# Performance work log

Hardware: AMD Instinct MI355X
Metric: run time of the kernel (lower is better)

## Reference

```python
import jax, jax.numpy as jnp
import numpy as np

TAU = 0.1

def setup_inputs() -> dict:
    key = jax.random.key(0)
    kZ, k1, k2 = jax.random.split(key, 3)
    N, D = 8192, 128
    scale = 1.0 / np.sqrt(D)
    return {
        "Z": jax.random.normal(kZ, (N, D), dtype=jnp.float32),
        "W1": jax.random.normal(k1, (D, D), dtype=jnp.float32) * scale,
        "b1": jnp.zeros((D,), dtype=jnp.float32),
        "W2": jax.random.normal(k2, (D, D), dtype=jnp.float32) * scale,
        "b2": jnp.zeros((D,), dtype=jnp.float32),
    }

def reference(Z, W1, b1, W2, b2):
    # DiffusivityTransform: 2-layer MLP with ReLU (torch Linear: x @ W.T + b;
    # here W1/W2 are stored already transposed as [in, out])
    t = jax.nn.relu(Z @ W1 + b1) @ W2 + b2          # [N, D]
    sim = t @ t.T                                     # [N, N]
    S = jax.nn.softmax(sim, axis=1)                   # row-stochastic [N, N]
    Z_prop = S @ Z                                    # [N, D]
    return Z + TAU * (Z_prop - Z)
```

## Files before the change

kernel.cpp:

```cpp
#include <hip/hip_runtime.h>

typedef _Float16 half_t;
typedef _Float16 hx8 __attribute__((ext_vector_type(8)));
typedef _Float16 hx4 __attribute__((ext_vector_type(4)));
typedef float fx4 __attribute__((ext_vector_type(4)));

#define LOG2E 1.44269504088896f
#define TAU 0.1f
#define NSPLIT 8

__global__ __launch_bounds__(256) void mlpz_kernel(
    const float* __restrict__ Z, const float* __restrict__ W1,
    const float* __restrict__ b1, const float* __restrict__ W2,
    const float* __restrict__ b2, half_t* __restrict__ T,
    half_t* __restrict__ Zth)
{
  __shared__ float Ztile[16*132];
  __shared__ half_t Hs[16*136];
  const int tid = threadIdx.x;
  const int w = tid >> 6, lane = tid & 63;
  const int q = lane >> 4, c = lane & 15;
  const int rb = blockIdx.x*16;

#pragma unroll
  for (int i=0;i<2;++i) {
    int fid = i*256 + tid;
    int r = fid >> 5, c4 = (fid & 31)*4;
    *(fx4*)(&Ztile[r*132 + c4]) = *(const fx4*)(Z + (size_t)(rb + r)*128 + c4);
  }
  __syncthreads();

  {
    const int d = tid & 127, h = tid >> 7;
    hx8 hv;
#pragma unroll
    for (int u=0;u<8;++u) hv[u] = (half_t)Ztile[(h*8 + u)*132 + d];
    *(hx8*)(Zth + (size_t)d*8192 + rb + h*8) = hv;
  }

  hx8 zb[4];
#pragma unroll
  for (int ks=0;ks<4;++ks) {
    fx4 a = *(const fx4*)(&Ztile[c*132 + ks*32 + q*8]);
    fx4 b = *(const fx4*)(&Ztile[c*132 + ks*32 + q*8 + 4]);
#pragma unroll
    for (int u=0;u<4;++u) { zb[ks][u] = (half_t)a[u]; zb[ks][4+u] = (half_t)b[u]; }
  }

#pragma unroll
  for (int m2=0;m2<2;++m2) {
    const int mt = w*2 + m2;
    fx4 acc = (fx4){0.f,0.f,0.f,0.f};
#pragma unroll
    for (int ks=0;ks<4;++ks) {
      hx8 aw;
#pragma unroll
      for (int j=0;j<8;++j)
        aw[j] = (half_t)W1[(size_t)(ks*32 + q*8 + j)*128 + mt*16 + c];
      acc = __builtin_amdgcn_mfma_f32_16x16x32_f16(aw, zb[ks], acc, 0,0,0);
    }
    fx4 bias = *(const fx4*)(b1 + mt*16 + 4*q);
    hx4 hv;
#pragma unroll
    for (int i=0;i<4;++i) {
      float h = acc[i] + bias[i];
      hv[i] = (half_t)(h > 0.f ? h : 0.f);
    }
    *(hx4*)(&Hs[c*136 + mt*16 + 4*q]) = hv;
  }
  __syncthreads();

  hx8 hb[4];
#pragma unroll
  for (int ks=0;ks<4;++ks) hb[ks] = *(const hx8*)(&Hs[c*136 + ks*32 + q*8]);
#pragma unroll
  for (int m2=0;m2<2;++m2) {
    const int mt = w*2 + m2;
    fx4 acc = (fx4){0.f,0.f,0.f,0.f};
#pragma unroll
    for (int ks=0;ks<4;++ks) {
      hx8 aw;
#pragma unroll
      for (int j=0;j<8;++j)
        aw[j] = (half_t)W2[(size_t)(ks*32 + q*8 + j)*128 + mt*16 + c];
      acc = __builtin_amdgcn_mfma_f32_16x16x32_f16(aw, hb[ks], acc, 0,0,0);
    }
    fx4 bias = *(const fx4*)(b2 + mt*16 + 4*q);
    hx4 tv;
#pragma unroll
    for (int i=0;i<4;++i) tv[i] = (half_t)(acc[i] + bias[i]);
    *(hx4*)(T + (size_t)(rb + c)*128 + mt*16 + 4*q) = tv;
  }
}

__global__ __launch_bounds__(256,2) void flash_kernel(
    const half_t* __restrict__ T, const half_t* __restrict__ Zt,
    half_t* __restrict__ Pacc, float* __restrict__ Pm, float* __restrict__ Pl)
{
  __shared__ half_t Tbuf[2][8*512];
  __shared__ half_t Zbuf[2][8*512];
  const int tid = threadIdx.x;
  const int w = tid >> 6, lane = tid & 63;
  const int q = lane >> 4, c = lane & 15;
  const int bx = blockIdx.x;
  const int qb = bx >> 3, kh = bx & 7;
  const int wrow = qb*128 + w*32;
  const int sw = (c & 3) * 8;

  hx8 bq[2][4];
#pragma unroll
  for (int nt=0;nt<2;++nt)
#pragma unroll
    for (int ks=0;ks<4;++ks)
      bq[nt][ks] = *(const hx8*)(T + (size_t)(wrow + nt*16 + c)*128 + ks*32 + q*8);

  fx4 oacc[8][2];
#pragma unroll
  for (int mtd=0;mtd<8;++mtd)
#pragma unroll
    for (int nt=0;nt<2;++nt) oacc[mtd][nt] = (fx4){0.f,0.f,0.f,0.f};
  float m_run[2] = {-1e30f,-1e30f};
  float l_run[2] = {0.f,0.f};

  const int kbase = kh*1024;

  auto issue_loads = [&](int kt0, int b) {
    if (w < 2) {
#pragma unroll
      for (int i=0;i<4;++i) {
        int f = w*4 + i, mt = f >> 2, ks = f & 3;
        const half_t* gp = T + (size_t)(kt0 + mt*16 + c)*128 + ks*32 + q*8;
        half_t* lp = &Tbuf[b][f*512 + lane*8];
        __builtin_amdgcn_global_load_lds(
            (const __attribute__((address_space(1))) void*)gp,
            (__attribute__((address_space(3))) void*)lp, 16, 0, 0);
      }
    } else {
#pragma unroll
      for (int i=0;i<4;++i) {
        int f2 = (w-2)*4 + i;
        const half_t* gp = Zt + (size_t)(f2*16 + c)*8192 + kt0 + q*8;
        half_t* lp = &Zbuf[b][f2*512 + lane*8];
        __builtin_amdgcn_global_load_lds(
            (const __attribute__((address_space(1))) void*)gp,
            (__attribute__((address_space(3))) void*)lp, 16, 0, 0);
      }
    }
  };

  issue_loads(kbase, 0);

  for (int t=0;t<32;++t) {
    const int cur = t & 1;
    __syncthreads();
    half_t* Tcur = Tbuf[cur];
    half_t* Zcur = Zbuf[cur];
    half_t* Psw  = &Tbuf[cur][w*1024];

    fx4 sacc[2][2];
#pragma unroll
    for (int mt=0;mt<2;++mt)
#pragma unroll
      for (int nt=0;nt<2;++nt) sacc[mt][nt] = (fx4){0.f,0.f,0.f,0.f};
#pragma unroll
    for (int ks=0;ks<4;++ks)
#pragma unroll
      for (int mt=0;mt<2;++mt) {
        hx8 ak = *(const hx8*)(&Tcur[(mt*4+ks)*512 + lane*8]);
        sacc[mt][0] = __builtin_amdgcn_mfma_f32_16x16x32_f16(ak, bq[0][ks], sacc[mt][0], 0,0,0);
        sacc[mt][1] = __builtin_amdgcn_mfma_f32_16x16x32_f16(ak, bq[1][ks], sacc[mt][1], 0,0,0);
      }

    hx4 pk[2][2];
#pragma unroll
    for (int nt=0;nt<2;++nt) {
      float mx = -1e30f;
#pragma unroll
      for (int mt=0;mt<2;++mt)
#pragma unroll
        for (int i=0;i<4;++i) mx = fmaxf(mx, sacc[mt][nt][i]);
      mx = fmaxf(mx, __shfl_xor(mx, 16, 64));
      mx = fmaxf(mx, __shfl_xor(mx, 32, 64));
      float mnew = fmaxf(m_run[nt], mx);
      float alpha = __builtin_amdgcn_exp2f((m_run[nt]-mnew)*LOG2E);
      m_run[nt] = mnew;
      float nb = mnew*LOG2E;
      float rs = 0.f;
#pragma unroll
      for (int mt=0;mt<2;++mt) {
#pragma unroll
        for (int i=0;i<4;++i) {
          float p = __builtin_amdgcn_exp2f(sacc[mt][nt][i]*LOG2E - nb);
          rs += p;
          pk[nt][mt][i] = (half_t)p;
        }
      }
      rs += __shfl_xor(rs, 16, 64);
      rs += __shfl_xor(rs, 32, 64);
      l_run[nt] = l_run[nt]*alpha + rs;
#pragma unroll
      for (int mtd=0;mtd<8;++mtd)
#pragma unroll
        for (int i=0;i<4;++i) oacc[mtd][nt][i] *= alpha;
    }

    __syncthreads();
    if (t < 31) issue_loads(kbase + (t+1)*32, cur ^ 1);

#pragma unroll
    for (int nt=0;nt<2;++nt)
#pragma unroll
      for (int mt=0;mt<2;++mt)
        *(hx4*)(&Psw[(nt*16 + c)*32 + ((mt*16 + 4*q) ^ sw)]) = pk[nt][mt];

    {
      hx8 bp0 = *(const hx8*)(&Psw[(c     )*32 + ((q*8) ^ sw)]);
      hx8 bp1 = *(const hx8*)(&Psw[(16 + c)*32 + ((q*8) ^ sw)]);
#pragma unroll
      for (int mtd=0;mtd<8;++mtd) {
        hx8 az = *(const hx8*)(&Zcur[mtd*512 + lane*8]);
        oacc[mtd][0] = __builtin_amdgcn_mfma_f32_16x16x32_f16(az, bp0, oacc[mtd][0], 0,0,0);
        oacc[mtd][1] = __builtin_amdgcn_mfma_f32_16x16x32_f16(az, bp1, oacc[mtd][1], 0,0,0);
      }
    }
  }

#pragma unroll
  for (int nt=0;nt<2;++nt) {
    float inv = 1.0f / l_run[nt];
    const size_t rowg = (size_t)(bx*128 + w*32 + nt*16 + c);
#pragma unroll
    for (int mtd=0;mtd<8;++mtd) {
      hx4 ov;
#pragma unroll
      for (int i=0;i<4;++i) ov[i] = (half_t)(oacc[mtd][nt][i]*inv);
      *(hx4*)(Pacc + rowg*128 + mtd*16 + 4*q) = ov;
    }
    if (q == 0) {
      Pm[rowg] = m_run[nt];
      Pl[rowg] = l_run[nt];
    }
  }
}

__global__ __launch_bounds__(256) void merge_kernel(
    const float* __restrict__ Z, const half_t* __restrict__ Pacc,
    const float* __restrict__ Pm, const float* __restrict__ Pl,
    float* __restrict__ out)
{
  const int th = blockIdx.x*256 + threadIdx.x;
  const int r = th >> 5, cg = th & 31;
  const int qb = r >> 7, rr = r & 127;
  float mk[NSPLIT], lk[NSPLIT];
  float M = -1e30f;
#pragma unroll
  for (int k=0;k<NSPLIT;++k) {
    int p = qb*NSPLIT + k;
    mk[k] = Pm[p*128 + rr];
    lk[k] = Pl[p*128 + rr];
    M = fmaxf(M, mk[k]);
  }
  float L = 0.f, wk[NSPLIT];
#pragma unroll
  for (int k=0;k<NSPLIT;++k) { wk[k] = lk[k]*__builtin_amdgcn_exp2f((mk[k]-M)*LOG2E); L += wk[k]; }
  float o0=0.f,o1=0.f,o2=0.f,o3=0.f;
#pragma unroll
  for (int k=0;k<NSPLIT;++k) {
    int p = qb*NSPLIT + k;
    hx4 v = *(const hx4*)(Pacc + ((size_t)p*128 + rr)*128 + cg*4);
    o0 += wk[k]*(float)v[0]; o1 += wk[k]*(float)v[1];
    o2 += wk[k]*(float)v[2]; o3 += wk[k]*(float)v[3];
  }
  float invL = 1.0f / L;
  fx4 zv = *(const fx4*)(Z + (size_t)r*128 + cg*4);
  fx4 res;
  res[0] = (1.f-TAU)*zv[0] + TAU*o0*invL;
  res[1] = (1.f-TAU)*zv[1] + TAU*o1*invL;
  res[2] = (1.f-TAU)*zv[2] + TAU*o2*invL;
  res[3] = (1.f-TAU)*zv[3] + TAU*o3*invL;
  *(fx4*)(out + (size_t)r*128 + cg*4) = res;
}

extern "C" void kernel_launch(void* const* d_in, const int* in_sizes, int n_in,
                              void* d_out, int out_size, void* d_ws, size_t ws_size,
                              hipStream_t stream) {
  const float* Z  = (const float*)d_in[0];
  const float* W1 = (const float*)d_in[1];
  const float* b1 = (const float*)d_in[2];
  const float* W2 = (const float*)d_in[3];
  const float* b2 = (const float*)d_in[4];
  float* out = (float*)d_out;

  char* ws = (char*)d_ws;
  const size_t NBLK = 64 * NSPLIT;
  half_t* Thi  = (half_t*)(ws);
  half_t* Zth  = (half_t*)(ws + (size_t)2*1024*1024);
  half_t* Pacc = (half_t*)(ws + (size_t)4*1024*1024);
  float*  Pm   = (float*)(ws + (size_t)4*1024*1024 + NBLK*128*128*2);
  float*  Pl   = Pm + NBLK*128;

  hipLaunchKernelGGL(mlpz_kernel,  dim3(512),  dim3(256), 0, stream, Z, W1, b1, W2, b2, Thi, Zth);
  hipLaunchKernelGGL(flash_kernel, dim3(NBLK), dim3(256), 0, stream, Thi, Zth, Pacc, Pm, Pl);
  hipLaunchKernelGGL(merge_kernel, dim3(1024), dim3(256), 0, stream, Z, Pacc, Pm, Pl, out);
}
```

Before: 138.9 us.

## Halve query rows per flash block to double grid size and add MFMA priority

Result: slower. 144.8 us (+4.2%).

```diff
diff --git a/kernel.cpp b/kernel.cpp
--- a/kernel.cpp
+++ b/kernel.cpp
@@ -104,23 +104,19 @@
   const int q = lane >> 4, c = lane & 15;
   const int bx = blockIdx.x;
   const int qb = bx >> 3, kh = bx & 7;
-  const int wrow = qb*128 + w*32;
-  const int sw = (c & 3) * 8;
-
-  hx8 bq[2][4];
-#pragma unroll
-  for (int nt=0;nt<2;++nt)
-#pragma unroll
-    for (int ks=0;ks<4;++ks)
-      bq[nt][ks] = *(const hx8*)(T + (size_t)(wrow + nt*16 + c)*128 + ks*32 + q*8);
-
-  fx4 oacc[8][2];
-#pragma unroll
-  for (int mtd=0;mtd<8;++mtd)
-#pragma unroll
-    for (int nt=0;nt<2;++nt) oacc[mtd][nt] = (fx4){0.f,0.f,0.f,0.f};
-  float m_run[2] = {-1e30f,-1e30f};
-  float l_run[2] = {0.f,0.f};
+  const int wrow = qb*64 + w*16;
+  const int sw = (c & 7) * 8;
+
+  hx8 bq[4];
+#pragma unroll
+  for (int ks=0;ks<4;++ks)
+    bq[ks] = *(const hx8*)(T + (size_t)(wrow + c)*128 + ks*32 + q*8);
+
+  fx4 oacc[8];
+#pragma unroll
+  for (int mtd=0;mtd<8;++mtd) oacc[mtd] = (fx4){0.f,0.f,0.f,0.f};
+  float m_run = -1e30f;
+  float l_run = 0.f;
 
   const int kbase = kh*1024;
 
@@ -157,89 +153,79 @@
     half_t* Zcur = Zbuf[cur];
     half_t* Psw  = &Tbuf[cur][w*1024];
 
-    fx4 sacc[2][2];
-#pragma unroll
-    for (int mt=0;mt<2;++mt)
-#pragma unroll
-      for (int nt=0;nt<2;++nt) sacc[mt][nt] = (fx4){0.f,0.f,0.f,0.f};
+    fx4 sacc[2];
+#pragma unroll
+    for (int mt=0;mt<2;++mt) sacc[mt] = (fx4){0.f,0.f,0.f,0.f};
+    __builtin_amdgcn_s_setprio(1);
 #pragma unroll
     for (int ks=0;ks<4;++ks)
 #pragma unroll
       for (int mt=0;mt<2;++mt) {
         hx8 ak = *(const hx8*)(&Tcur[(mt*4+ks)*512 + lane*8]);
-        sacc[mt][0] = __builtin_amdgcn_mfma_f32_16x16x32_f16(ak, bq[0][ks], sacc[mt][0], 0,0,0);
-        sacc[mt][1] = __builtin_amdgcn_mfma_f32_16x16x32_f16(ak, bq[1][ks], sacc[mt][1], 0,0,0);
-      }
-
-    hx4 pk[2][2];
-#pragma unroll
-    for (int nt=0;nt<2;++nt) {
-      float mx = -1e30f;
-#pragma unroll
-      for (int mt=0;mt<2;++mt)
-#pragma unroll
-        for (int i=0;i<4;++i) mx = fmaxf(mx, sacc[mt][nt][i]);
-      mx = fmaxf(mx, __shfl_xor(mx, 16, 64));
-      mx = fmaxf(mx, __shfl_xor(mx, 32, 64));
-      float mnew = fmaxf(m_run[nt], mx);
-      float alpha = __builtin_amdgcn_exp2f((m_run[nt]-mnew)*LOG2E);
-      m_run[nt] = mnew;
-      float nb = mnew*LOG2E;
-      float rs = 0.f;
-#pragma unroll
-      for (int mt=0;mt<2;++mt) {
-#pragma unroll
-        for (int i=0;i<4;++i) {
-          float p = __builtin_amdgcn_exp2f(sacc[mt][nt][i]*LOG2E - nb);
-          rs += p;
-          pk[nt][mt][i] = (half_t)p;
-        }
-      }
-      rs += __shfl_xor(rs, 16, 64);
-      rs += __shfl_xor(rs, 32, 64);
-      l_run[nt] = l_run[nt]*alpha + rs;
-#pragma unroll
-      for (int mtd=0;mtd<8;++mtd)
-#pragma unroll
-        for (int i=0;i<4;++i) oacc[mtd][nt][i] *= alpha;
-    }
+        sacc[mt] = __builtin_amdgcn_mfma_f32_16x16x32_f16(ak, bq[ks], sacc[mt], 0,0,0);
+      }
+    __builtin_amdgcn_s_setprio(0);
+
+    float mx = -1e30f;
+#pragma unroll
+    for (int mt=0;mt<2;++mt)
+#pragma unroll
+      for (int i=0;i<4;++i) mx = fmaxf(mx, sacc[mt][i]);
+    mx = fmaxf(mx, __shfl_xor(mx, 16, 64));
+    mx = fmaxf(mx, __shfl_xor(mx, 32, 64));
+    float mnew = fmaxf(m_run, mx);
+    float alpha = __builtin_amdgcn_exp2f((m_run - mnew)*LOG2E);
+    m_run = mnew;
+    float nb = mnew*LOG2E;
+    float rs = 0.f;
+    hx4 pk[2];
+#pragma unroll
+    for (int mt=0;mt<2;++mt)
+#pragma unroll
+      for (int i=0;i<4;++i) {
+        float p = __builtin_amdgcn_exp2f(sacc[mt][i]*LOG2E - nb);
+        rs += p;
+        pk[mt][i] = (half_t)p;
+      }
+    rs += __shfl_xor(rs, 16, 64);
+    rs += __shfl_xor(rs, 32, 64);
+    l_run = l_run*alpha + rs;
+#pragma unroll
+    for (int mtd=0;mtd<8;++mtd)
+#pragma unroll
+      for (int i=0;i<4;++i) oacc[mtd][i] *= alpha;
 
     __syncthreads();
     if (t < 31) issue_loads(kbase + (t+1)*32, cur ^ 1);
 
 #pragma unroll
-    for (int nt=0;nt<2;++nt)
-#pragma unroll
-      for (int mt=0;mt<2;++mt)
-        *(hx4*)(&Psw[(nt*16 + c)*32 + ((mt*16 + 4*q) ^ sw)]) = pk[nt][mt];
+    for (int mt=0;mt<2;++mt)
+      *(hx4*)(&Psw[c*64 + ((mt*16 + 4*q) ^ sw)]) = pk[mt];
 
     {
-      hx8 bp0 = *(const hx8*)(&Psw[(c     )*32 + ((q*8) ^ sw)]);
-      hx8 bp1 = *(const hx8*)(&Psw[(16 + c)*32 + ((q*8) ^ sw)]);
+      hx8 bp = *(const hx8*)(&Psw[c*64 + ((q*8) ^ sw)]);
+      __builtin_amdgcn_s_setprio(1);
 #pragma unroll
       for (int mtd=0;mtd<8;++mtd) {
         hx8 az = *(const hx8*)(&Zcur[mtd*512 + lane*8]);
-        oacc[mtd][0] = __builtin_amdgcn_mfma_f32_16x16x32_f16(az, bp0, oacc[mtd][0], 0,0,0);
-        oacc[mtd][1] = __builtin_amdgcn_mfma_f32_16x16x32_f16(az, bp1, oacc[mtd][1], 0,0,0);
-      }
-    }
-  }
-
-#pragma unroll
-  for (int nt=0;nt<2;++nt) {
-    float inv = 1.0f / l_run[nt];
-    const size_t rowg = (size_t)(bx*128 + w*32 + nt*16 + c);
-#pragma unroll
-    for (int mtd=0;mtd<8;++mtd) {
-      hx4 ov;
-#pragma unroll
-      for (int i=0;i<4;++i) ov[i] = (half_t)(oacc[mtd][nt][i]*inv);
-      *(hx4*)(Pacc + rowg*128 + mtd*16 + 4*q) = ov;
-    }
-    if (q == 0) {
-      Pm[rowg] = m_run[nt];
-      Pl[rowg] = l_run[nt];
-    }
+        oacc[mtd] = __builtin_amdgcn_mfma_f32_16x16x32_f16(az, bp, oacc[mtd], 0,0,0);
+      }
+      __builtin_amdgcn_s_setprio(0);
+    }
+  }
+
+  float inv = 1.0f / l_run;
+  const size_t prow = (size_t)(((qb >> 1)*8 + kh)*128 + (qb & 1)*64 + w*16 + c);
+#pragma unroll
+  for (int mtd=0;mtd<8;++mtd) {
+    hx4 ov;
+#pragma unroll
+    for (int i=0;i<4;++i) ov[i] = (half_t)(oacc[mtd][i]*inv);
+    *(hx4*)(Pacc + prow*128 + mtd*16 + 4*q) = ov;
+  }
+  if (q == 0) {
+    Pm[prow] = m_run;
+    Pl[prow] = l_run;
   }
 }
 
@@ -300,6 +286,6 @@
   float*  Pl   = Pm + NBLK*128;
 
   hipLaunchKernelGGL(mlpz_kernel,  dim3(512),  dim3(256), 0, stream, Z, W1, b1, W2, b2, Thi, Zth);
-  hipLaunchKernelGGL(flash_kernel, dim3(NBLK), dim3(256), 0, stream, Thi, Zth, Pacc, Pm, Pl);
+  hipLaunchKernelGGL(flash_kernel, dim3(128*NSPLIT), dim3(256), 0, stream, Thi, Zth, Pacc, Pm, Pl);
   hipLaunchKernelGGL(merge_kernel, dim3(1024), dim3(256), 0, stream, Z, Pacc, Pm, Pl, out);
 }
```
